# Kernel tuning notes

Measured on AMD Instinct MI355X. Metric: run time of the kernel, lower is better.

## Reference

```python
import jax, jax.numpy as jnp
import numpy as np

BATCH = 16
D_MODEL = 384
STATE = 64          # state_dim
D_INNER = 384       # ssd_expand * d_model
H = 64
W = 64


def setup_inputs() -> dict:
    key = jax.random.key(0)
    ks = jax.random.split(key, 6)
    x = jax.random.normal(ks[0], (BATCH, D_MODEL, H * W), jnp.float32)
    # 1x1 Conv1d weights stored as 2D matrices [out_ch, in_ch]
    W_bcdt = jax.random.normal(ks[1], (3 * STATE, D_MODEL), jnp.float32) / np.sqrt(D_MODEL).astype(np.float32)
    # depthwise 3x3 conv, groups = 3*STATE -> kernel [3S, 1, 3, 3]
    W_dw = jax.random.normal(ks[2], (3 * STATE, 1, 3, 3), jnp.float32) / 3.0
    W_hz = jax.random.normal(ks[3], (2 * D_INNER, D_MODEL), jnp.float32) / np.sqrt(D_MODEL).astype(np.float32)
    W_out = jax.random.normal(ks[4], (D_MODEL, D_INNER), jnp.float32) / np.sqrt(D_INNER).astype(np.float32)
    A_param = jax.random.uniform(ks[5], (STATE,), jnp.float32, 1.0, 16.0)
    D_param = jnp.ones((1,), jnp.float32)
    return {"x": x, "W_bcdt": W_bcdt, "W_dw": W_dw, "W_hz": W_hz,
            "W_out": W_out, "A_param": A_param, "D_param": D_param,
            "size_h": H, "size_w": W}


def reference(x, W_bcdt, W_dw, W_hz, W_out, A_param, D_param, size_h, size_w):
    b, d, L = x.shape
    S = A_param.shape[0]
    # BCdt_proj: 1x1 conv1d == matmul over channel dim -> [b, 3S, L]
    bcdt = jnp.einsum('od,bdl->bol', W_bcdt, x)
    # depthwise 3x3 conv over the spatial view [b, 3S, H, W]
    xhw = bcdt.reshape(b, 3 * S, size_h, size_w)
    xhw = jax.lax.conv_general_dilated(
        xhw, W_dw, window_strides=(1, 1), padding='SAME',
        dimension_numbers=('NCHW', 'OIHW', 'NCHW'),
        feature_group_count=3 * S)
    bcdt = xhw.reshape(b, 3 * S, L)
    Bm, Cm, dt = jnp.split(bcdt, 3, axis=1)          # each [b, S, L]
    # softmax over the sequence dim with learned A offset
    A = jax.nn.softmax(dt + A_param[None, :, None], axis=-1)
    AB = A * Bm                                       # [b, S, L]
    h = jnp.einsum('bdl,bsl->bds', x, AB)             # x @ AB^T -> [b, d, S]
    hz = jnp.einsum('od,bds->bos', W_hz, h)           # hz_proj -> [b, 2*d_inner, S]
    h1, z = jnp.split(hz, 2, axis=1)                  # each [b, d_inner, S]
    hgate = h1 * jax.nn.silu(z) + h1 * D_param[0]
    hout = jnp.einsum('oe,bes->bos', W_out, hgate)    # out_proj -> [b, d, S]
    y = jnp.einsum('bds,bsl->bdl', hout, Cm)          # h @ C -> [b, d, L]
    y = y.reshape(b, d, size_h, size_w)
    return (y, hout)
```

## Files before the change

kernel.cpp:

```cpp
#include <hip/hip_runtime.h>

typedef unsigned short u16;
typedef short s16x8 __attribute__((ext_vector_type(8)));
typedef float f32x4 __attribute__((ext_vector_type(4)));

#define NB 16
#define DMODEL 384
#define SDIM 64
#define LSEQ 4096
#define C3S 192

__device__ __forceinline__ float b2f(u16 u) {
    union { unsigned int i; float f; } v; v.i = ((unsigned int)u) << 16; return v.f;
}
__device__ __forceinline__ u16 f2b(float f) {
    union { float ff; unsigned int i; } v; v.ff = f;
    unsigned int x = v.i;
    unsigned int r = (x + 0x7fffu + ((x >> 16) & 1u)) >> 16;
    return (u16)r;
}

__global__ __launch_bounds__(256) void kcvt(const float* __restrict__ x,
                                            u16* __restrict__ xbT) {
    __shared__ __align__(16) u16 T[64][72];
    const int t = threadIdx.x;
    const int l0 = blockIdx.x * 64;
    const int d0 = blockIdx.y * 64;
    const int b = blockIdx.z;
    const int dr = t >> 2;
    const int lo = (t & 3) * 16;
    const float* xp = x + ((size_t)(b * DMODEL + d0 + dr)) * LSEQ + l0 + lo;
    float4 x0 = *reinterpret_cast<const float4*>(xp + 0);
    float4 x1 = *reinterpret_cast<const float4*>(xp + 4);
    float4 x2 = *reinterpret_cast<const float4*>(xp + 8);
    float4 x3 = *reinterpret_cast<const float4*>(xp + 12);
    s16x8 va, vb;
    va[0] = (short)f2b(x0.x); va[1] = (short)f2b(x0.y); va[2] = (short)f2b(x0.z); va[3] = (short)f2b(x0.w);
    va[4] = (short)f2b(x1.x); va[5] = (short)f2b(x1.y); va[6] = (short)f2b(x1.z); va[7] = (short)f2b(x1.w);
    vb[0] = (short)f2b(x2.x); vb[1] = (short)f2b(x2.y); vb[2] = (short)f2b(x2.z); vb[3] = (short)f2b(x2.w);
    vb[4] = (short)f2b(x3.x); vb[5] = (short)f2b(x3.y); vb[6] = (short)f2b(x3.z); vb[7] = (short)f2b(x3.w);
    *reinterpret_cast<s16x8*>(&T[dr][lo + 0]) = va;
    *reinterpret_cast<s16x8*>(&T[dr][lo + 8]) = vb;
    __syncthreads();
    const int lr = t >> 2;
    const int dof = (t & 3) * 16;
    s16x8 wa, wb;
    #pragma unroll
    for (int j = 0; j < 8; ++j) {
        wa[j] = (short)T[dof + j][lr];
        wb[j] = (short)T[dof + 8 + j][lr];
    }
    u16* xtp = xbT + ((size_t)(b * LSEQ + l0 + lr)) * DMODEL + d0 + dof;
    *reinterpret_cast<s16x8*>(xtp + 0) = wa;
    *reinterpret_cast<s16x8*>(xtp + 8) = wb;
}

__global__ __launch_bounds__(256) void k1_mfma(const u16* __restrict__ xbT,
                                               const float* __restrict__ Wb,
                                               u16* __restrict__ rawb) {
    __shared__ __align__(16) short As[64 * 40];
    __shared__ __align__(16) short Bs[256 * 40];
    const int t = threadIdx.x;
    const int l0 = blockIdx.x * 256;
    const int o0 = blockIdx.y * 64;
    const int b = blockIdx.z;
    const int lane = t & 63;
    const int w = t >> 6;
    const int wm = w >> 1, wn = w & 1;
    const int lm = lane & 15, kg = lane >> 4;
    f32x4 acc[2][8];
    #pragma unroll
    for (int i = 0; i < 2; ++i)
        #pragma unroll
        for (int j = 0; j < 8; ++j) acc[i][j] = (f32x4){0.f, 0.f, 0.f, 0.f};

    const int arow = t >> 2;
    const int aoff = (t & 3) * 8;
    const float* wp = Wb + (size_t)(o0 + arow) * DMODEL + aoff;
    const u16* bp = xbT + ((size_t)(b * LSEQ + l0)) * DMODEL;

    for (int kc = 0; kc < DMODEL; kc += 32) {
        float4 w0 = *reinterpret_cast<const float4*>(wp + kc);
        float4 w1 = *reinterpret_cast<const float4*>(wp + kc + 4);
        s16x8 av;
        av[0] = (short)f2b(w0.x); av[1] = (short)f2b(w0.y); av[2] = (short)f2b(w0.z); av[3] = (short)f2b(w0.w);
        av[4] = (short)f2b(w1.x); av[5] = (short)f2b(w1.y); av[6] = (short)f2b(w1.z); av[7] = (short)f2b(w1.w);
        *reinterpret_cast<s16x8*>(&As[arow * 40 + aoff]) = av;
        #pragma unroll
        for (int i = 0; i < 4; ++i) {
            int c = t + i * 256;
            int brow = c >> 2;
            int boff = (c & 3) * 8;
            s16x8 bv = *reinterpret_cast<const s16x8*>(bp + (size_t)brow * DMODEL + kc + boff);
            *reinterpret_cast<s16x8*>(&Bs[brow * 40 + boff]) = bv;
        }
        __syncthreads();
        s16x8 af[2], bf[8];
        #pragma unroll
        for (int i = 0; i < 2; ++i)
            af[i] = *reinterpret_cast<s16x8*>(&As[(wm * 32 + i * 16 + lm) * 40 + kg * 8]);
        #pragma unroll
        for (int j = 0; j < 8; ++j)
            bf[j] = *reinterpret_cast<s16x8*>(&Bs[(wn * 128 + j * 16 + lm) * 40 + kg * 8]);
        #pragma unroll
        for (int i = 0; i < 2; ++i)
            #pragma unroll
            for (int j = 0; j < 8; ++j)
                acc[i][j] = __builtin_amdgcn_mfma_f32_16x16x32_bf16(af[i], bf[j], acc[i][j], 0, 0, 0);
        __syncthreads();
    }
    #pragma unroll
    for (int i = 0; i < 2; ++i) {
        #pragma unroll
        for (int j = 0; j < 8; ++j) {
            #pragma unroll
            for (int r = 0; r < 4; ++r) {
                int o = o0 + wm * 32 + i * 16 + kg * 4 + r;
                int l = l0 + wn * 128 + j * 16 + lm;
                rawb[((size_t)b * C3S + o) * LSEQ + l] = f2b(acc[i][j][r]);
            }
        }
    }
}

__global__ __launch_bounds__(256) void k23_ab(const u16* __restrict__ rawb,
                                              const float* __restrict__ Wdw,
                                              const float* __restrict__ Ap,
                                              u16* __restrict__ AB,
                                              u16* __restrict__ CMB) {
    __shared__ __align__(16) u16 chB[LSEQ];
    __shared__ __align__(16) u16 chC[LSEQ];
    __shared__ __align__(16) u16 chT[LSEQ];
    __shared__ float red[4];
    const int t = threadIdx.x;
    const int s = blockIdx.x;
    const int b = blockIdx.y;
    const u16* rB = rawb + ((size_t)b * C3S + s) * LSEQ;
    const u16* rC = rawb + ((size_t)b * C3S + 64 + s) * LSEQ;
    const u16* rT = rawb + ((size_t)b * C3S + 128 + s) * LSEQ;
    #pragma unroll
    for (int i = 0; i < 2; ++i) {
        int c8 = (t + i * 256) * 8;
        *reinterpret_cast<s16x8*>(&chB[c8]) = *reinterpret_cast<const s16x8*>(rB + c8);
        *reinterpret_cast<s16x8*>(&chC[c8]) = *reinterpret_cast<const s16x8*>(rC + c8);
        *reinterpret_cast<s16x8*>(&chT[c8]) = *reinterpret_cast<const s16x8*>(rT + c8);
    }
    __syncthreads();
    float wB[9], wC[9], wT[9];
    #pragma unroll
    for (int k = 0; k < 9; ++k) {
        wB[k] = Wdw[s * 9 + k];
        wC[k] = Wdw[(64 + s) * 9 + k];
        wT[k] = Wdw[(128 + s) * 9 + k];
    }
    const float a = Ap[s];
    u16* cmp = CMB + ((size_t)b * SDIM + s) * LSEQ;
    float vB[16], vT[16];
    float m = -3.0e38f;
    #pragma unroll
    for (int i = 0; i < 16; ++i) {
        int idx = t + i * 256;
        int row = idx >> 6, col = idx & 63;
        float aB = 0.f, aC = 0.f, aT = 0.f;
        #pragma unroll
        for (int dy = -1; dy <= 1; ++dy) {
            int r = row + dy;
            if (r < 0 || r > 63) continue;
            #pragma unroll
            for (int dx = -1; dx <= 1; ++dx) {
                int cc = col + dx;
                if (cc < 0 || cc > 63) continue;
                int p = r * 64 + cc;
                int wi = (dy + 1) * 3 + (dx + 1);
                aB = fmaf(wB[wi], b2f(chB[p]), aB);
                aC = fmaf(wC[wi], b2f(chC[p]), aC);
                aT = fmaf(wT[wi], b2f(chT[p]), aT);
            }
        }
        cmp[idx] = f2b(aC);
        vB[i] = aB;
        vT[i] = aT + a;
        m = fmaxf(m, vT[i]);
    }
    #pragma unroll
    for (int off = 32; off; off >>= 1) m = fmaxf(m, __shfl_xor(m, off));
    if ((t & 63) == 0) red[t >> 6] = m;
    __syncthreads();
    m = fmaxf(fmaxf(red[0], red[1]), fmaxf(red[2], red[3]));
    __syncthreads();
    float sum = 0.f;
    #pragma unroll
    for (int i = 0; i < 16; ++i) {
        vT[i] = expf(vT[i] - m);
        sum += vT[i];
    }
    #pragma unroll
    for (int off = 32; off; off >>= 1) sum += __shfl_xor(sum, off);
    if ((t & 63) == 0) red[t >> 6] = sum;
    __syncthreads();
    sum = red[0] + red[1] + red[2] + red[3];
    const float inv = 1.0f / sum;
    u16* op = AB + ((size_t)b * SDIM + s) * LSEQ;
    #pragma unroll
    for (int i = 0; i < 16; ++i) {
        int idx = t + i * 256;
        op[idx] = f2b(vT[i] * inv * vB[i]);
    }
}

__global__ __launch_bounds__(256) void kcmT(const u16* __restrict__ CMB,
                                            u16* __restrict__ CmT) {
    __shared__ __align__(16) u16 T[64][72];
    const int t = threadIdx.x;
    const int l0 = blockIdx.x * 64;
    const int b = blockIdx.y;
    const int sr = t >> 2;
    const int lo = (t & 3) * 16;
    const u16* ip = CMB + ((size_t)(b * SDIM + sr)) * LSEQ + l0 + lo;
    s16x8 va = *reinterpret_cast<const s16x8*>(ip);
    s16x8 vb = *reinterpret_cast<const s16x8*>(ip + 8);
    *reinterpret_cast<s16x8*>(&T[sr][lo + 0]) = va;
    *reinterpret_cast<s16x8*>(&T[sr][lo + 8]) = vb;
    __syncthreads();
    const int lr = t >> 2;
    const int sof = (t & 3) * 16;
    s16x8 wa, wb;
    #pragma unroll
    for (int j = 0; j < 8; ++j) {
        wa[j] = (short)T[sof + j][lr];
        wb[j] = (short)T[sof + 8 + j][lr];
    }
    u16* op = CmT + ((size_t)(b * LSEQ + l0 + lr)) * SDIM + sof;
    *reinterpret_cast<s16x8*>(op + 0) = wa;
    *reinterpret_cast<s16x8*>(op + 8) = wb;
}

__global__ __launch_bounds__(256) void k4_mfma(const float* __restrict__ x,
                                               const u16* __restrict__ ABu,
                                               float* __restrict__ hpart) {
    __shared__ __align__(16) short As[64 * 40];
    __shared__ __align__(16) short Bs[64 * 40];
    const int t = threadIdx.x;
    const int d0 = blockIdx.x * 64;
    const int kc = blockIdx.y;
    const int b = blockIdx.z;
    const int lane = t & 63;
    const int w = t >> 6;
    const int wm = w >> 1, wn = w & 1;
    const int lm = lane & 15, kg = lane >> 4;
    const int arow = t >> 2;
    const int aoff = (t & 3) * 8;
    const float* ap = x + ((size_t)(b * DMODEL + d0 + arow)) * LSEQ + kc * 1024 + aoff;
    const u16* bp = ABu + ((size_t)(b * SDIM + arow)) * LSEQ + kc * 1024 + aoff;
    f32x4 acc[2][2];
    #pragma unroll
    for (int i = 0; i < 2; ++i)
        #pragma unroll
        for (int j = 0; j < 2; ++j) acc[i][j] = (f32x4){0.f, 0.f, 0.f, 0.f};

    for (int ks = 0; ks < 1024; ks += 32) {
        float4 a0 = *reinterpret_cast<const float4*>(ap + ks);
        float4 a1 = *reinterpret_cast<const float4*>(ap + ks + 4);
        s16x8 av;
        av[0] = (short)f2b(a0.x); av[1] = (short)f2b(a0.y); av[2] = (short)f2b(a0.z); av[3] = (short)f2b(a0.w);
        av[4] = (short)f2b(a1.x); av[5] = (short)f2b(a1.y); av[6] = (short)f2b(a1.z); av[7] = (short)f2b(a1.w);
        s16x8 bv = *reinterpret_cast<const s16x8*>(bp + ks);
        *reinterpret_cast<s16x8*>(&As[arow * 40 + aoff]) = av;
        *reinterpret_cast<s16x8*>(&Bs[arow * 40 + aoff]) = bv;
        __syncthreads();
        s16x8 af[2], bf[2];
        #pragma unroll
        for (int i = 0; i < 2; ++i) {
            af[i] = *reinterpret_cast<s16x8*>(&As[(wm * 32 + i * 16 + lm) * 40 + kg * 8]);
            bf[i] = *reinterpret_cast<s16x8*>(&Bs[(wn * 32 + i * 16 + lm) * 40 + kg * 8]);
        }
        #pragma unroll
        for (int i = 0; i < 2; ++i)
            #pragma unroll
            for (int j = 0; j < 2; ++j)
                acc[i][j] = __builtin_amdgcn_mfma_f32_16x16x32_bf16(af[i], bf[j], acc[i][j], 0, 0, 0);
        __syncthreads();
    }
    #pragma unroll
    for (int i = 0; i < 2; ++i) {
        #pragma unroll
        for (int j = 0; j < 2; ++j) {
            int d = d0 + wm * 32 + i * 16 + kg * 4;
            int s = wn * 32 + j * 16 + lm;
            float* p = hpart + (size_t)kc * (1024 * DMODEL) + ((size_t)b * 64 + s) * DMODEL + d;
            *reinterpret_cast<f32x4*>(p) = acc[i][j];
        }
    }
}

__global__ __launch_bounds__(256) void k4r(const float* __restrict__ hp,
                                           u16* __restrict__ htb) {
    const int i = (blockIdx.x * 256 + threadIdx.x) * 4;
    const int N = 1024 * DMODEL;
    float4 v0 = *reinterpret_cast<const float4*>(hp + i);
    float4 v1 = *reinterpret_cast<const float4*>(hp + N + i);
    float4 v2 = *reinterpret_cast<const float4*>(hp + 2 * N + i);
    float4 v3 = *reinterpret_cast<const float4*>(hp + 3 * N + i);
    ushort4 o;
    o.x = f2b(v0.x + v1.x + v2.x + v3.x);
    o.y = f2b(v0.y + v1.y + v2.y + v3.y);
    o.z = f2b(v0.z + v1.z + v2.z + v3.z);
    o.w = f2b(v0.w + v1.w + v2.w + v3.w);
    *reinterpret_cast<ushort4*>(htb + i) = o;
}

__global__ __launch_bounds__(256) void k5hz(const u16* __restrict__ HTB,
                                            const float* __restrict__ Whz,
                                            float* __restrict__ HZT) {
    __shared__ __align__(16) short As[64 * 40];
    __shared__ __align__(16) short Bs[64 * 40];
    const int t = threadIdx.x;
    const int m0 = blockIdx.x * 64;
    const int n0 = blockIdx.y * 64;
    const int lane = t & 63;
    const int w = t >> 6;
    const int wm = w >> 1, wn = w & 1;
    const int lm = lane & 15, kg = lane >> 4;
    const int arow = t >> 2;
    const int aoff = (t & 3) * 8;
    const u16* apg = HTB + (size_t)(m0 + arow) * DMODEL + aoff;
    const float* bpg = Whz + (size_t)(n0 + arow) * DMODEL + aoff;
    f32x4 acc[2][2];
    #pragma unroll
    for (int i = 0; i < 2; ++i)
        #pragma unroll
        for (int j = 0; j < 2; ++j) acc[i][j] = (f32x4){0.f, 0.f, 0.f, 0.f};

    for (int kc = 0; kc < DMODEL; kc += 32) {
        s16x8 av = *reinterpret_cast<const s16x8*>(apg + kc);
        float4 b0 = *reinterpret_cast<const float4*>(bpg + kc);
        float4 b1 = *reinterpret_cast<const float4*>(bpg + kc + 4);
        s16x8 bv;
        bv[0] = (short)f2b(b0.x); bv[1] = (short)f2b(b0.y); bv[2] = (short)f2b(b0.z); bv[3] = (short)f2b(b0.w);
        bv[4] = (short)f2b(b1.x); bv[5] = (short)f2b(b1.y); bv[6] = (short)f2b(b1.z); bv[7] = (short)f2b(b1.w);
        *reinterpret_cast<s16x8*>(&As[arow * 40 + aoff]) = av;
        *reinterpret_cast<s16x8*>(&Bs[arow * 40 + aoff]) = bv;
        __syncthreads();
        s16x8 af[2], bf[2];
        #pragma unroll
        for (int i = 0; i < 2; ++i) {
            af[i] = *reinterpret_cast<s16x8*>(&As[(wm * 32 + i * 16 + lm) * 40 + kg * 8]);
            bf[i] = *reinterpret_cast<s16x8*>(&Bs[(wn * 32 + i * 16 + lm) * 40 + kg * 8]);
        }
        #pragma unroll
        for (int i = 0; i < 2; ++i)
            #pragma unroll
            for (int j = 0; j < 2; ++j)
                acc[i][j] = __builtin_amdgcn_mfma_f32_16x16x32_bf16(af[i], bf[j], acc[i][j], 0, 0, 0);
        __syncthreads();
    }
    #pragma unroll
    for (int i = 0; i < 2; ++i) {
        #pragma unroll
        for (int j = 0; j < 2; ++j) {
            #pragma unroll
            for (int r = 0; r < 4; ++r) {
                int bs = m0 + wm * 32 + i * 16 + kg * 4 + r;
                int o = n0 + wn * 32 + j * 16 + lm;
                HZT[(size_t)bs * 768 + o] = acc[i][j][r];
            }
        }
    }
}

__global__ __launch_bounds__(256) void k5g(const float* __restrict__ HZT,
                                           const float* __restrict__ Dp,
                                           u16* __restrict__ HGT) {
    const int i = (blockIdx.x * 256 + threadIdx.x) * 4;
    const int bs = i / DMODEL, d = i - bs * DMODEL;
    const float* p = HZT + (size_t)bs * 768 + d;
    float4 h1 = *reinterpret_cast<const float4*>(p);
    float4 z  = *reinterpret_cast<const float4*>(p + DMODEL);
    const float Dv = Dp[0];
    ushort4 o;
    o.x = f2b(h1.x * (z.x / (1.f + expf(-z.x)) + Dv));
    o.y = f2b(h1.y * (z.y / (1.f + expf(-z.y)) + Dv));
    o.z = f2b(h1.z * (z.z / (1.f + expf(-z.z)) + Dv));
    o.w = f2b(h1.w * (z.w / (1.f + expf(-z.w)) + Dv));
    *reinterpret_cast<ushort4*>(HGT + i) = o;
}

__global__ __launch_bounds__(256) void k5ho(const u16* __restrict__ HGT,
                                            const float* __restrict__ Wout,
                                            float* __restrict__ ho,
                                            u16* __restrict__ hob) {
    __shared__ __align__(16) short As[64 * 40];
    __shared__ __align__(16) short Bs[64 * 40];
    const int t = threadIdx.x;
    const int m0 = blockIdx.x * 64;
    const int n0 = blockIdx.y * 64;
    const int lane = t & 63;
    const int w = t >> 6;
    const int wm = w >> 1, wn = w & 1;
    const int lm = lane & 15, kg = lane >> 4;
    const int arow = t >> 2;
    const int aoff = (t & 3) * 8;
    const u16* apg = HGT + (size_t)(m0 + arow) * DMODEL + aoff;
    const float* bpg = Wout + (size_t)(n0 + arow) * DMODEL + aoff;
    f32x4 acc[2][2];
    #pragma unroll
    for (int i = 0; i < 2; ++i)
        #pragma unroll
        for (int j = 0; j < 2; ++j) acc[i][j] = (f32x4){0.f, 0.f, 0.f, 0.f};

    for (int kc = 0; kc < DMODEL; kc += 32) {
        s16x8 av = *reinterpret_cast<const s16x8*>(apg + kc);
        float4 b0 = *reinterpret_cast<const float4*>(bpg + kc);
        float4 b1 = *reinterpret_cast<const float4*>(bpg + kc + 4);
        s16x8 bv;
        bv[0] = (short)f2b(b0.x); bv[1] = (short)f2b(b0.y); bv[2] = (short)f2b(b0.z); bv[3] = (short)f2b(b0.w);
        bv[4] = (short)f2b(b1.x); bv[5] = (short)f2b(b1.y); bv[6] = (short)f2b(b1.z); bv[7] = (short)f2b(b1.w);
        *reinterpret_cast<s16x8*>(&As[arow * 40 + aoff]) = av;
        *reinterpret_cast<s16x8*>(&Bs[arow * 40 + aoff]) = bv;
        __syncthreads();
        s16x8 af[2], bf[2];
        #pragma unroll
        for (int i = 0; i < 2; ++i) {
            af[i] = *reinterpret_cast<s16x8*>(&As[(wm * 32 + i * 16 + lm) * 40 + kg * 8]);
            bf[i] = *reinterpret_cast<s16x8*>(&Bs[(wn * 32 + i * 16 + lm) * 40 + kg * 8]);
        }
        #pragma unroll
        for (int i = 0; i < 2; ++i)
            #pragma unroll
            for (int j = 0; j < 2; ++j)
                acc[i][j] = __builtin_amdgcn_mfma_f32_16x16x32_bf16(af[i], bf[j], acc[i][j], 0, 0, 0);
        __syncthreads();
    }
    #pragma unroll
    for (int i = 0; i < 2; ++i) {
        #pragma unroll
        for (int j = 0; j < 2; ++j) {
            int bs = m0 + wm * 32 + i * 16 + kg * 4;
            int b = bs >> 6, s = bs & 63;
            int o = n0 + wn * 32 + j * 16 + lm;
            size_t idx = ((size_t)b * DMODEL + o) * SDIM + s;
            *reinterpret_cast<f32x4*>(ho + idx) = acc[i][j];
            ushort4 u;
            u.x = f2b(acc[i][j][0]); u.y = f2b(acc[i][j][1]);
            u.z = f2b(acc[i][j][2]); u.w = f2b(acc[i][j][3]);
            *reinterpret_cast<ushort4*>(hob + idx) = u;
        }
    }
}

__global__ __launch_bounds__(256) void k6_mfma(const u16* __restrict__ CmT,
                                               const u16* __restrict__ hob,
                                               float* __restrict__ y) {
    const int t = threadIdx.x;
    const int l0 = blockIdx.x * 128;
    const int d0 = blockIdx.y * 128;
    const int b = blockIdx.z;
    const int lane = t & 63;
    const int w = t >> 6;
    const int wm = w >> 1, wn = w & 1;
    const int lm = lane & 15, kg = lane >> 4;
    const u16* hp = hob + (size_t)b * DMODEL * SDIM;
    const u16* cp = CmT + (size_t)b * LSEQ * SDIM;
    s16x8 af[4][2], bf[4][2];
    #pragma unroll
    for (int i = 0; i < 4; ++i)
        #pragma unroll
        for (int ks = 0; ks < 2; ++ks)
            af[i][ks] = *reinterpret_cast<const s16x8*>(
                hp + (size_t)(d0 + wm * 64 + i * 16 + lm) * SDIM + ks * 32 + kg * 8);
    #pragma unroll
    for (int j = 0; j < 4; ++j)
        #pragma unroll
        for (int ks = 0; ks < 2; ++ks)
            bf[j][ks] = *reinterpret_cast<const s16x8*>(
                cp + (size_t)(l0 + wn * 64 + j * 16 + lm) * SDIM + ks * 32 + kg * 8);
    f32x4 acc[4][4];
    #pragma unroll
    for (int i = 0; i < 4; ++i)
        #pragma unroll
        for (int j = 0; j < 4; ++j) acc[i][j] = (f32x4){0.f, 0.f, 0.f, 0.f};
    #pragma unroll
    for (int ks = 0; ks < 2; ++ks)
        #pragma unroll
        for (int i = 0; i < 4; ++i)
            #pragma unroll
            for (int j = 0; j < 4; ++j)
                acc[i][j] = __builtin_amdgcn_mfma_f32_16x16x32_bf16(af[i][ks], bf[j][ks], acc[i][j], 0, 0, 0);
    float* yp = y + (size_t)b * DMODEL * LSEQ;
    #pragma unroll
    for (int i = 0; i < 4; ++i) {
        #pragma unroll
        for (int j = 0; j < 4; ++j) {
            #pragma unroll
            for (int r = 0; r < 4; ++r) {
                int d = d0 + wm * 64 + i * 16 + kg * 4 + r;
                int l = l0 + wn * 64 + j * 16 + lm;
                yp[(size_t)d * LSEQ + l] = acc[i][j][r];
            }
        }
    }
}

extern "C" void kernel_launch(void* const* d_in, const int* in_sizes, int n_in,
                              void* d_out, int out_size, void* d_ws, size_t ws_size,
                              hipStream_t stream) {
    const float* x    = (const float*)d_in[0];
    const float* Wb   = (const float*)d_in[1];
    const float* Wdw  = (const float*)d_in[2];
    const float* Whz  = (const float*)d_in[3];
    const float* Wout = (const float*)d_in[4];
    const float* Ap   = (const float*)d_in[5];
    const float* Dp   = (const float*)d_in[6];

    float* out = (float*)d_out;
    const size_t YSIZE = (size_t)NB * DMODEL * LSEQ;

    u16*   RAWB   = (u16*)out;
    u16*   XBT    = (u16*)(out + 8388608);
    u16*   CMB    = (u16*)(out + 8388608);
    u16*   ABu    = (u16*)(out + 20971520);
    float* HPART  = out;
    u16*   HTB    = (u16*)(out + 1572864);
    float* HZT    = out + 1769472;
    u16*   HGT    = (u16*)(out + 2555904);
    float* HO     = out + YSIZE;
    u16*   CmT    = (u16*)d_ws;
    u16*   HOB    = (u16*)d_ws + 4194304;

    kcvt   <<<dim3(64, 6, NB), 256, 0, stream>>>(x, XBT);
    k1_mfma<<<dim3(16, 3, NB), 256, 0, stream>>>(XBT, Wb, RAWB);
    k23_ab <<<dim3(SDIM, NB), 256, 0, stream>>>(RAWB, Wdw, Ap, ABu, CMB);
    kcmT   <<<dim3(64, NB), 256, 0, stream>>>(CMB, CmT);
    k4_mfma<<<dim3(6, 4, NB), 256, 0, stream>>>(x, ABu, HPART);
    k4r    <<<dim3(384), 256, 0, stream>>>(HPART, HTB);
    k5hz   <<<dim3(16, 12), 256, 0, stream>>>(HTB, Whz, HZT);
    k5g    <<<dim3(384), 256, 0, stream>>>(HZT, Dp, HGT);
    k5ho   <<<dim3(16, 6), 256, 0, stream>>>(HGT, Wout, HO, HOB);
    k6_mfma<<<dim3(32, 3, NB), 256, 0, stream>>>(CmT, HOB, out);
}
```

Measured before the change: 149.5 us.

## Fuse x bf16 transpose into BCdt projection GEMM and halve k4 tile

```diff
diff --git a/kernel.cpp b/kernel.cpp
--- a/kernel.cpp
+++ b/kernel.cpp
@@ -20,103 +20,83 @@
     return (u16)r;
 }
 
-__global__ __launch_bounds__(256) void kcvt(const float* __restrict__ x,
-                                            u16* __restrict__ xbT) {
-    __shared__ __align__(16) u16 T[64][72];
-    const int t = threadIdx.x;
-    const int l0 = blockIdx.x * 64;
-    const int d0 = blockIdx.y * 64;
-    const int b = blockIdx.z;
-    const int dr = t >> 2;
-    const int lo = (t & 3) * 16;
-    const float* xp = x + ((size_t)(b * DMODEL + d0 + dr)) * LSEQ + l0 + lo;
-    float4 x0 = *reinterpret_cast<const float4*>(xp + 0);
-    float4 x1 = *reinterpret_cast<const float4*>(xp + 4);
-    float4 x2 = *reinterpret_cast<const float4*>(xp + 8);
-    float4 x3 = *reinterpret_cast<const float4*>(xp + 12);
-    s16x8 va, vb;
-    va[0] = (short)f2b(x0.x); va[1] = (short)f2b(x0.y); va[2] = (short)f2b(x0.z); va[3] = (short)f2b(x0.w);
-    va[4] = (short)f2b(x1.x); va[5] = (short)f2b(x1.y); va[6] = (short)f2b(x1.z); va[7] = (short)f2b(x1.w);
-    vb[0] = (short)f2b(x2.x); vb[1] = (short)f2b(x2.y); vb[2] = (short)f2b(x2.z); vb[3] = (short)f2b(x2.w);
-    vb[4] = (short)f2b(x3.x); vb[5] = (short)f2b(x3.y); vb[6] = (short)f2b(x3.z); vb[7] = (short)f2b(x3.w);
-    *reinterpret_cast<s16x8*>(&T[dr][lo + 0]) = va;
-    *reinterpret_cast<s16x8*>(&T[dr][lo + 8]) = vb;
-    __syncthreads();
-    const int lr = t >> 2;
-    const int dof = (t & 3) * 16;
-    s16x8 wa, wb;
-    #pragma unroll
-    for (int j = 0; j < 8; ++j) {
-        wa[j] = (short)T[dof + j][lr];
-        wb[j] = (short)T[dof + 8 + j][lr];
-    }
-    u16* xtp = xbT + ((size_t)(b * LSEQ + l0 + lr)) * DMODEL + d0 + dof;
-    *reinterpret_cast<s16x8*>(xtp + 0) = wa;
-    *reinterpret_cast<s16x8*>(xtp + 8) = wb;
-}
-
-__global__ __launch_bounds__(256) void k1_mfma(const u16* __restrict__ xbT,
-                                               const float* __restrict__ Wb,
-                                               u16* __restrict__ rawb) {
-    __shared__ __align__(16) short As[64 * 40];
-    __shared__ __align__(16) short Bs[256 * 40];
-    const int t = threadIdx.x;
-    const int l0 = blockIdx.x * 256;
-    const int o0 = blockIdx.y * 64;
-    const int b = blockIdx.z;
+__global__ __launch_bounds__(512, 4) void k01_mfma(const float* __restrict__ x,
+                                                   const float* __restrict__ Wb,
+                                                   u16* __restrict__ rawb) {
+    __shared__ __align__(16) u16  XR[32 * 136];
+    __shared__ __align__(16) short As[192 * 40];
+    __shared__ __align__(16) short Bs[128 * 40];
+    const int t = threadIdx.x;
+    const int l0 = blockIdx.x * 128;
+    const int b = blockIdx.y;
     const int lane = t & 63;
     const int w = t >> 6;
     const int wm = w >> 1, wn = w & 1;
     const int lm = lane & 15, kg = lane >> 4;
-    f32x4 acc[2][8];
-    #pragma unroll
-    for (int i = 0; i < 2; ++i)
-        #pragma unroll
-        for (int j = 0; j < 8; ++j) acc[i][j] = (f32x4){0.f, 0.f, 0.f, 0.f};
-
-    const int arow = t >> 2;
-    const int aoff = (t & 3) * 8;
-    const float* wp = Wb + (size_t)(o0 + arow) * DMODEL + aoff;
-    const u16* bp = xbT + ((size_t)(b * LSEQ + l0)) * DMODEL;
+
+    f32x4 acc[3][4];
+    #pragma unroll
+    for (int i = 0; i < 3; ++i)
+        #pragma unroll
+        for (int j = 0; j < 4; ++j) acc[i][j] = (f32x4){0.f, 0.f, 0.f, 0.f};
+
+    const int xr = t >> 4;
+    const int xli = (t & 15) * 8;
+    const int bl = t >> 2;
+    const int bdq = (t & 3) * 8;
 
     for (int kc = 0; kc < DMODEL; kc += 32) {
-        float4 w0 = *reinterpret_cast<const float4*>(wp + kc);
-        float4 w1 = *reinterpret_cast<const float4*>(wp + kc + 4);
-        s16x8 av;
-        av[0] = (short)f2b(w0.x); av[1] = (short)f2b(w0.y); av[2] = (short)f2b(w0.z); av[3] = (short)f2b(w0.w);
-        av[4] = (short)f2b(w1.x); av[5] = (short)f2b(w1.y); av[6] = (short)f2b(w1.z); av[7] = (short)f2b(w1.w);
-        *reinterpret_cast<s16x8*>(&As[arow * 40 + aoff]) = av;
-        #pragma unroll
-        for (int i = 0; i < 4; ++i) {
-            int c = t + i * 256;
-            int brow = c >> 2;
-            int boff = (c & 3) * 8;
-            s16x8 bv = *reinterpret_cast<const s16x8*>(bp + (size_t)brow * DMODEL + kc + boff);
-            *reinterpret_cast<s16x8*>(&Bs[brow * 40 + boff]) = bv;
-        }
-        __syncthreads();
-        s16x8 af[2], bf[8];
-        #pragma unroll
-        for (int i = 0; i < 2; ++i)
-            af[i] = *reinterpret_cast<s16x8*>(&As[(wm * 32 + i * 16 + lm) * 40 + kg * 8]);
-        #pragma unroll
-        for (int j = 0; j < 8; ++j)
-            bf[j] = *reinterpret_cast<s16x8*>(&Bs[(wn * 128 + j * 16 + lm) * 40 + kg * 8]);
-        #pragma unroll
-        for (int i = 0; i < 2; ++i)
-            #pragma unroll
-            for (int j = 0; j < 8; ++j)
+        if (t < 192) {
+            const float* wp = Wb + (size_t)t * DMODEL + kc;
+            #pragma unroll
+            for (int c = 0; c < 4; ++c) {
+                float4 w0 = *reinterpret_cast<const float4*>(wp + c * 8);
+                float4 w1 = *reinterpret_cast<const float4*>(wp + c * 8 + 4);
+                s16x8 av;
+                av[0] = (short)f2b(w0.x); av[1] = (short)f2b(w0.y); av[2] = (short)f2b(w0.z); av[3] = (short)f2b(w0.w);
+                av[4] = (short)f2b(w1.x); av[5] = (short)f2b(w1.y); av[6] = (short)f2b(w1.z); av[7] = (short)f2b(w1.w);
+                *reinterpret_cast<s16x8*>(&As[t * 40 + c * 8]) = av;
+            }
+        }
+        {
+            const float* xp = x + ((size_t)(b * DMODEL + kc + xr)) * LSEQ + l0 + xli;
+            float4 x0 = *reinterpret_cast<const float4*>(xp);
+            float4 x1 = *reinterpret_cast<const float4*>(xp + 4);
+            s16x8 v;
+            v[0] = (short)f2b(x0.x); v[1] = (short)f2b(x0.y); v[2] = (short)f2b(x0.z); v[3] = (short)f2b(x0.w);
+            v[4] = (short)f2b(x1.x); v[5] = (short)f2b(x1.y); v[6] = (short)f2b(x1.z); v[7] = (short)f2b(x1.w);
+            *reinterpret_cast<s16x8*>(&XR[xr * 136 + xli]) = v;
+        }
+        __syncthreads();
+        {
+            s16x8 v;
+            #pragma unroll
+            for (int j = 0; j < 8; ++j) v[j] = (short)XR[(bdq + j) * 136 + bl];
+            *reinterpret_cast<s16x8*>(&Bs[bl * 40 + bdq]) = v;
+        }
+        __syncthreads();
+        s16x8 af[3], bf[4];
+        #pragma unroll
+        for (int i = 0; i < 3; ++i)
+            af[i] = *reinterpret_cast<s16x8*>(&As[(wm * 48 + i * 16 + lm) * 40 + kg * 8]);
+        #pragma unroll
+        for (int j = 0; j < 4; ++j)
+            bf[j] = *reinterpret_cast<s16x8*>(&Bs[(wn * 64 + j * 16 + lm) * 40 + kg * 8]);
+        #pragma unroll
+        for (int i = 0; i < 3; ++i)
+            #pragma unroll
+            for (int j = 0; j < 4; ++j)
                 acc[i][j] = __builtin_amdgcn_mfma_f32_16x16x32_bf16(af[i], bf[j], acc[i][j], 0, 0, 0);
         __syncthreads();
     }
     #pragma unroll
-    for (int i = 0; i < 2; ++i) {
-        #pragma unroll
-        for (int j = 0; j < 8; ++j) {
+    for (int i = 0; i < 3; ++i) {
+        #pragma unroll
+        for (int j = 0; j < 4; ++j) {
             #pragma unroll
             for (int r = 0; r < 4; ++r) {
-                int o = o0 + wm * 32 + i * 16 + kg * 4 + r;
-                int l = l0 + wn * 128 + j * 16 + lm;
+                int o = wm * 48 + i * 16 + kg * 4 + r;
+                int l = l0 + wn * 64 + j * 16 + lm;
                 rawb[((size_t)b * C3S + o) * LSEQ + l] = f2b(acc[i][j][r]);
             }
         }
@@ -238,10 +218,10 @@
 __global__ __launch_bounds__(256) void k4_mfma(const float* __restrict__ x,
                                                const u16* __restrict__ ABu,
                                                float* __restrict__ hpart) {
-    __shared__ __align__(16) short As[64 * 40];
+    __shared__ __align__(16) short As[32 * 40];
     __shared__ __align__(16) short Bs[64 * 40];
     const int t = threadIdx.x;
-    const int d0 = blockIdx.x * 64;
+    const int d0 = blockIdx.x * 32;
     const int kc = blockIdx.y;
     const int b = blockIdx.z;
     const int lane = t & 63;
@@ -250,46 +230,37 @@
     const int lm = lane & 15, kg = lane >> 4;
     const int arow = t >> 2;
     const int aoff = (t & 3) * 8;
-    const float* ap = x + ((size_t)(b * DMODEL + d0 + arow)) * LSEQ + kc * 1024 + aoff;
+    const float* ap = x + ((size_t)(b * DMODEL + d0 + (arow & 31))) * LSEQ + kc * 1024 + aoff;
     const u16* bp = ABu + ((size_t)(b * SDIM + arow)) * LSEQ + kc * 1024 + aoff;
-    f32x4 acc[2][2];
-    #pragma unroll
-    for (int i = 0; i < 2; ++i)
-        #pragma unroll
-        for (int j = 0; j < 2; ++j) acc[i][j] = (f32x4){0.f, 0.f, 0.f, 0.f};
+    f32x4 acc[2];
+    acc[0] = (f32x4){0.f, 0.f, 0.f, 0.f};
+    acc[1] = (f32x4){0.f, 0.f, 0.f, 0.f};
 
     for (int ks = 0; ks < 1024; ks += 32) {
-        float4 a0 = *reinterpret_cast<const float4*>(ap + ks);
-        float4 a1 = *reinterpret_cast<const float4*>(ap + ks + 4);
-        s16x8 av;
-        av[0] = (short)f2b(a0.x); av[1] = (short)f2b(a0.y); av[2] = (short)f2b(a0.z); av[3] = (short)f2b(a0.w);
-        av[4] = (short)f2b(a1.x); av[5] = (short)f2b(a1.y); av[6] = (short)f2b(a1.z); av[7] = (short)f2b(a1.w);
+        if (t < 128) {
+            float4 a0 = *reinterpret_cast<const float4*>(ap + ks);
+            float4 a1 = *reinterpret_cast<const float4*>(ap + ks + 4);
+            s16x8 av;
+            av[0] = (short)f2b(a0.x); av[1] = (short)f2b(a0.y); av[2] = (short)f2b(a0.z); av[3] = (short)f2b(a0.w);
+            av[4] = (short)f2b(a1.x); av[5] = (short)f2b(a1.y); av[6] = (short)f2b(a1.z); av[7] = (short)f2b(a1.w);
+            *reinterpret_cast<s16x8*>(&As[arow * 40 + aoff]) = av;
+        }
         s16x8 bv = *reinterpret_cast<const s16x8*>(bp + ks);
-        *reinterpret_cast<s16x8*>(&As[arow * 40 + aoff]) = av;
         *reinterpret_cast<s16x8*>(&Bs[arow * 40 + aoff]) = bv;
         __syncthreads();
-        s16x8 af[2], bf[2];
-        #pragma unroll
-        for (int i = 0; i < 2; ++i) {
-            af[i] = *reinterpret_cast<s16x8*>(&As[(wm * 32 + i * 16 + lm) * 40 + kg * 8]);
-            bf[i] = *reinterpret_cast<s16x8*>(&Bs[(wn * 32 + i * 16 + lm) * 40 + kg * 8]);
-        }
-        #pragma unroll
-        for (int i = 0; i < 2; ++i)
-            #pragma unroll
-            for (int j = 0; j < 2; ++j)
-                acc[i][j] = __builtin_amdgcn_mfma_f32_16x16x32_bf16(af[i], bf[j], acc[i][j], 0, 0, 0);
-        __syncthreads();
-    }
-    #pragma unroll
-    for (int i = 0; i < 2; ++i) {
-        #pragma unroll
-        for (int j = 0; j < 2; ++j) {
-            int d = d0 + wm * 32 + i * 16 + kg * 4;
-            int s = wn * 32 + j * 16 + lm;
-            float* p = hpart + (size_t)kc * (1024 * DMODEL) + ((size_t)b * 64 + s) * DMODEL + d;
-            *reinterpret_cast<f32x4*>(p) = acc[i][j];
-        }
+        s16x8 af = *reinterpret_cast<s16x8*>(&As[(wm * 16 + lm) * 40 + kg * 8]);
+        s16x8 bf0 = *reinterpret_cast<s16x8*>(&Bs[(wn * 32 + lm) * 40 + kg * 8]);
+        s16x8 bf1 = *reinterpret_cast<s16x8*>(&Bs[(wn * 32 + 16 + lm) * 40 + kg * 8]);
+        acc[0] = __builtin_amdgcn_mfma_f32_16x16x32_bf16(af, bf0, acc[0], 0, 0, 0);
+        acc[1] = __builtin_amdgcn_mfma_f32_16x16x32_bf16(af, bf1, acc[1], 0, 0, 0);
+        __syncthreads();
+    }
+    #pragma unroll
+    for (int j = 0; j < 2; ++j) {
+        int d = d0 + wm * 16 + kg * 4;
+        int s = wn * 32 + j * 16 + lm;
+        float* p = hpart + (size_t)kc * (1024 * DMODEL) + ((size_t)b * 64 + s) * DMODEL + d;
+        *reinterpret_cast<f32x4*>(p) = acc[j];
     }
 }
 
@@ -516,7 +487,6 @@
     const size_t YSIZE = (size_t)NB * DMODEL * LSEQ;
 
     u16*   RAWB   = (u16*)out;
-    u16*   XBT    = (u16*)(out + 8388608);
     u16*   CMB    = (u16*)(out + 8388608);
     u16*   ABu    = (u16*)(out + 20971520);
     float* HPART  = out;
@@ -527,14 +497,13 @@
     u16*   CmT    = (u16*)d_ws;
     u16*   HOB    = (u16*)d_ws + 4194304;
 
-    kcvt   <<<dim3(64, 6, NB), 256, 0, stream>>>(x, XBT);
-    k1_mfma<<<dim3(16, 3, NB), 256, 0, stream>>>(XBT, Wb, RAWB);
-    k23_ab <<<dim3(SDIM, NB), 256, 0, stream>>>(RAWB, Wdw, Ap, ABu, CMB);
-    kcmT   <<<dim3(64, NB), 256, 0, stream>>>(CMB, CmT);
-    k4_mfma<<<dim3(6, 4, NB), 256, 0, stream>>>(x, ABu, HPART);
-    k4r    <<<dim3(384), 256, 0, stream>>>(HPART, HTB);
-    k5hz   <<<dim3(16, 12), 256, 0, stream>>>(HTB, Whz, HZT);
-    k5g    <<<dim3(384), 256, 0, stream>>>(HZT, Dp, HGT);
-    k5ho   <<<dim3(16, 6), 256, 0, stream>>>(HGT, Wout, HO, HOB);
-    k6_mfma<<<dim3(32, 3, NB), 256, 0, stream>>>(CmT, HOB, out);
-}
+    k01_mfma<<<dim3(32, NB), 512, 0, stream>>>(x, Wb, RAWB);
+    k23_ab  <<<dim3(SDIM, NB), 256, 0, stream>>>(RAWB, Wdw, Ap, ABu, CMB);
+    kcmT    <<<dim3(64, NB), 256, 0, stream>>>(CMB, CmT);
+    k4_mfma <<<dim3(12, 4, NB), 256, 0, stream>>>(x, ABu, HPART);
+    k4r     <<<dim3(384), 256, 0, stream>>>(HPART, HTB);
+    k5hz    <<<dim3(16, 12), 256, 0, stream>>>(HTB, Whz, HZT);
+    k5g     <<<dim3(384), 256, 0, stream>>>(HZT, Dp, HGT);
+    k5ho    <<<dim3(16, 6), 256, 0, stream>>>(HGT, Wout, HO, HOB);
+    k6_mfma <<<dim3(32, 3, NB), 256, 0, stream>>>(CmT, HOB, out);
+}
```

Measured after the change: 141.7 us. 1.06x faster.
